# Performance work log

Measured on AMD Instinct MI355X. Metric: run time of the kernel, lower is better.

The kernel has to match this reference:

```python
import jax, jax.numpy as jnp
import numpy as np

NUM_FEATURES = 5
HIDDEN = 64
NUM_CLASSES = 5
N_NODES = 100000
N_EDGES = 1600000


def setup_inputs() -> dict:
    key = jax.random.key(0)
    ks = jax.random.split(key, 8)
    x = jax.random.normal(ks[0], (N_NODES, 4, NUM_FEATURES), dtype=jnp.float32)
    edge_index = jax.random.randint(ks[1], (2, N_EDGES), 0, N_NODES, dtype=jnp.int64)
    batch = jnp.zeros((N_NODES,), dtype=jnp.int64)
    # GCNConv layer 1: 5 -> 64, layer 2: 64 -> 64, output Linear: 64 -> 5
    W1 = jax.random.normal(ks[2], (NUM_FEATURES, HIDDEN), dtype=jnp.float32) / np.sqrt(NUM_FEATURES)
    b1 = jnp.zeros((HIDDEN,), dtype=jnp.float32)
    W2 = jax.random.normal(ks[3], (HIDDEN, HIDDEN), dtype=jnp.float32) / np.sqrt(HIDDEN)
    b2 = jnp.zeros((HIDDEN,), dtype=jnp.float32)
    Wout = jax.random.normal(ks[4], (HIDDEN, NUM_CLASSES), dtype=jnp.float32) / np.sqrt(HIDDEN)
    bout = jnp.zeros((NUM_CLASSES,), dtype=jnp.float32)
    return {"x": x, "edge_index": edge_index, "batch": batch,
            "W1": W1, "b1": b1, "W2": W2, "b2": b2, "Wout": Wout, "bout": bout}


def reference(x, edge_index, batch, W1, b1, W2, b2, Wout, bout):
    N = x.shape[0]
    src, dst = edge_index[0], edge_index[1]
    # GCN symmetric normalization with self-loops: deg counts incoming edges + self loop
    deg = jax.ops.segment_sum(jnp.ones(src.shape, jnp.float32), dst, num_segments=N) + 1.0
    dinv_sqrt = jax.lax.rsqrt(deg)
    norm = dinv_sqrt[src] * dinv_sqrt[dst]            # [E]
    self_norm = (1.0 / deg)[:, None]                  # self-loop weight deg^-1

    def gcn_conv(h, W, b):
        h = h @ W                                     # [N, out]
        agg = jax.ops.segment_sum(h[src] * norm[:, None], dst, num_segments=N)
        return agg + h * self_norm + b

    h = jax.nn.relu(gcn_conv(x[:, -1, :], W1, b1))    # [N, HIDDEN]
    h = jax.nn.relu(gcn_conv(h, W2, b2))              # [N, HIDDEN]
    return jax.nn.softmax(h @ Wout + bout, axis=1)    # [N, 5]
```

## Files before the change

### kernel.cpp

```cpp
#include <hip/hip_runtime.h>
#include <hip/hip_fp16.h>

#define HID 64
#define NF 5
#define NC 5

#define WSH 8
#define WINN 256
#define NBMAX 512
#define SRCB 17
#define NBLK_FILL 160

__global__ void k_zero_i32(int* __restrict__ p, int n) {
    int i = blockIdx.x * blockDim.x + threadIdx.x;
    if (i < n) p[i] = 0;
}


__global__ __launch_bounds__(256) void k_bcount(const int* __restrict__ dst, int E, int chunk,
                                                int nb, int* __restrict__ bcount) {
    __shared__ int cnt[NBMAX];
    for (int i = threadIdx.x; i < nb; i += 256) cnt[i] = 0;
    __syncthreads();
    int c0 = blockIdx.x * chunk;
    int c1 = c0 + chunk; if (c1 > E) c1 = E;
    for (int i = c0 + threadIdx.x; i < c1; i += 256)
        atomicAdd(&cnt[dst[i] >> WSH], 1);
    __syncthreads();
    for (int i = threadIdx.x; i < nb; i += 256) {
        int v = cnt[i];
        if (v) atomicAdd(&bcount[i], v);
    }
}

__global__ __launch_bounds__(512) void k_bscan2(const int* __restrict__ bcount, int nb, int N,
                                                int* __restrict__ bbase, int* __restrict__ bcursor,
                                                int* __restrict__ offsets) {
    __shared__ int s[512];
    int t = threadIdx.x;
    int v = (t < nb) ? bcount[t] : 0;
    s[t] = v;
    __syncthreads();
    for (int o = 1; o < 512; o <<= 1) {
        int u = (t >= o) ? s[t - o] : 0;
        __syncthreads();
        s[t] += u;
        __syncthreads();
    }
    if (t < nb) { bbase[t] = s[t] - v; bcursor[t] = s[t] - v; }
    if (t == nb - 1) { bbase[nb] = s[t]; offsets[N] = s[t]; }
}

__global__ __launch_bounds__(256) void k_bfill(const int* __restrict__ src,
                                               const int* __restrict__ dst, int E, int chunk,
                                               int nb, int* __restrict__ bcursor,
                                               unsigned int* __restrict__ pairbuf) {
    __shared__ int cnt[NBMAX];
    __shared__ int wcur[NBMAX];
    for (int i = threadIdx.x; i < nb; i += 256) cnt[i] = 0;
    __syncthreads();
    int c0 = blockIdx.x * chunk;
    int c1 = c0 + chunk; if (c1 > E) c1 = E;
    for (int i = c0 + threadIdx.x; i < c1; i += 256)
        atomicAdd(&cnt[dst[i] >> WSH], 1);
    __syncthreads();
    for (int i = threadIdx.x; i < nb; i += 256) {
        int v = cnt[i];
        wcur[i] = v ? atomicAdd(&bcursor[i], v) : 0;
    }
    __syncthreads();
    for (int i = c0 + threadIdx.x; i < c1; i += 256) {
        int d = dst[i];
        int b = d >> WSH;
        int p = atomicAdd(&wcur[b], 1);
        pairbuf[p] = ((unsigned)(d & (WINN - 1)) << SRCB) | (unsigned)src[i];
    }
}

__global__ __launch_bounds__(WINN) void k_csr(const unsigned int* __restrict__ pairbuf,
                                              const int* __restrict__ bbase, int N,
                                              const float* __restrict__ x,
                                              int* __restrict__ offsets,
                                              int* __restrict__ csr_src,
                                              float* __restrict__ dinv,
                                              float* __restrict__ xs) {
    int b = blockIdx.x, t = threadIdx.x;
    int winStart = b << WSH;
    int rbeg = bbase[b], rend = bbase[b + 1];
    __shared__ int deg[WINN];
    __shared__ int cur[WINN];
    __shared__ int s[WINN];
    deg[t] = 0;
    __syncthreads();
    for (int p = rbeg + t; p < rend; p += WINN)
        atomicAdd(&deg[pairbuf[p] >> SRCB], 1);
    __syncthreads();
    int v = deg[t];
    s[t] = v;
    __syncthreads();
    for (int o = 1; o < WINN; o <<= 1) {
        int u = (t >= o) ? s[t - o] : 0;
        __syncthreads();
        s[t] += u;
        __syncthreads();
    }
    int node = winStart + t;
    if (node < N) {
        int base = rbeg + s[t] - v;
        offsets[node] = base;
        cur[t] = base;
        float dv = rsqrtf((float)v + 1.0f);
        dinv[node] = dv;
        const float* xr = x + (size_t)node * (4 * NF) + 3 * NF;
#pragma unroll
        for (int k = 0; k < NF; ++k) xs[(size_t)node * NF + k] = xr[k] * dv;
    }
    __syncthreads();
    for (int p = rbeg + t; p < rend; p += WINN) {
        unsigned u = pairbuf[p];
        int dl = u >> SRCB;
        int sn = u & ((1u << SRCB) - 1);
        int pos = atomicAdd(&cur[dl], 1);
        csr_src[pos] = sn;
    }
}


__global__ __launch_bounds__(256) void k_aggX(const float* __restrict__ xs,
                                              const float* __restrict__ W1,
                                              const int* __restrict__ offsets,
                                              const int* __restrict__ csr_src,
                                              const float* __restrict__ dinv,
                                              const float* __restrict__ b1,
                                              __half* __restrict__ g1, int N) {
    int wid = (blockIdx.x * blockDim.x + threadIdx.x) >> 6;
    int lane = threadIdx.x & 63;
    int g = lane >> 3;
    int f = lane & 7;
    float w0 = W1[0 * HID + lane], w1 = W1[1 * HID + lane], w2 = W1[2 * HID + lane],
          w3 = W1[3 * HID + lane], w4 = W1[4 * HID + lane];
    if (wid >= N) return;
    int e0 = offsets[wid], e1 = offsets[wid + 1];
    bool fa = (f < NF);
    float acc = 0.f;
    int ee = e0 + g;
    int s = (ee < e1) ? csr_src[ee] : -1;
    for (int e = e0; e < e1; e += 8) {
        int cs = s;
        int en = e + 8 + g;
        s = (en < e1) ? csr_src[en] : -1;
        if (cs >= 0 && fa) acc += xs[(size_t)cs * NF + f];
    }
    if (g == 0 && fa) acc += xs[(size_t)wid * NF + f];
    acc += __shfl_xor(acc, 8, 64);
    acc += __shfl_xor(acc, 16, 64);
    acc += __shfl_xor(acc, 32, 64);
    float a0 = __shfl(acc, 0, 8), a1 = __shfl(acc, 1, 8), a2 = __shfl(acc, 2, 8),
          a3 = __shfl(acc, 3, 8), a4 = __shfl(acc, 4, 8);
    float dv = dinv[wid];
    float sres = a0 * w0 + a1 * w1 + a2 * w2 + a3 * w3 + a4 * w4;
    float r = fmaxf(fmaf(dv, sres, b1[lane]), 0.f) * dv;
    g1[(size_t)wid * HID + lane] = __float2half(r);
}

__global__ __launch_bounds__(256) void k_aggG(const __half* __restrict__ g1,
                                              const int* __restrict__ offsets,
                                              const int* __restrict__ csr_src,
                                              const float* __restrict__ dinv,
                                              float* __restrict__ aggH, int N) {
    int wid = (blockIdx.x * blockDim.x + threadIdx.x) >> 6;
    if (wid >= N) return;
    int lane = threadIdx.x & 63;
    int g = lane >> 3;
    int f8 = (lane & 7) << 3;
    int e0 = offsets[wid], e1 = offsets[wid + 1];
    float acc[8];
#pragma unroll
    for (int i = 0; i < 8; ++i) acc[i] = 0.f;
    int ee = e0 + g;
    int s = (ee < e1) ? csr_src[ee] : -1;
    for (int e = e0; e < e1; e += 8) {
        int cs = s;
        int en = e + 8 + g;
        s = (en < e1) ? csr_src[en] : -1;
        if (cs >= 0) {
            float4 raw = *reinterpret_cast<const float4*>(g1 + (size_t)cs * HID + f8);
            float2 p0 = __half22float2(*reinterpret_cast<__half2*>(&raw.x));
            float2 p1 = __half22float2(*reinterpret_cast<__half2*>(&raw.y));
            float2 p2 = __half22float2(*reinterpret_cast<__half2*>(&raw.z));
            float2 p3 = __half22float2(*reinterpret_cast<__half2*>(&raw.w));
            acc[0] += p0.x; acc[1] += p0.y; acc[2] += p1.x; acc[3] += p1.y;
            acc[4] += p2.x; acc[5] += p2.y; acc[6] += p3.x; acc[7] += p3.y;
        }
    }
#pragma unroll
    for (int o = 8; o < 64; o <<= 1) {
#pragma unroll
        for (int i = 0; i < 8; ++i) acc[i] += __shfl_xor(acc[i], o, 64);
    }
    if (lane < 8) {
        float4 raw = *reinterpret_cast<const float4*>(g1 + (size_t)wid * HID + f8);
        float2 p0 = __half22float2(*reinterpret_cast<__half2*>(&raw.x));
        float2 p1 = __half22float2(*reinterpret_cast<__half2*>(&raw.y));
        float2 p2 = __half22float2(*reinterpret_cast<__half2*>(&raw.z));
        float2 p3 = __half22float2(*reinterpret_cast<__half2*>(&raw.w));
        float dv = dinv[wid];
        float4 r0, r1;
        r0.x = dv * (acc[0] + p0.x); r0.y = dv * (acc[1] + p0.y);
        r0.z = dv * (acc[2] + p1.x); r0.w = dv * (acc[3] + p1.y);
        r1.x = dv * (acc[4] + p2.x); r1.y = dv * (acc[5] + p2.y);
        r1.z = dv * (acc[6] + p3.x); r1.w = dv * (acc[7] + p3.y);
        float4* dst4 = reinterpret_cast<float4*>(aggH + (size_t)wid * HID + f8);
        dst4[0] = r0;
        dst4[1] = r1;
    }
}

__global__ __launch_bounds__(256) void k_fuse(const float* __restrict__ aggH,
                                              const float* __restrict__ W2,
                                              const float* __restrict__ b2,
                                              const float* __restrict__ Wout,
                                              const float* __restrict__ bout,
                                              float* __restrict__ out, int N) {
    __shared__ float4 sh4[64][17];
    __shared__ float4 sW4[64 * 16];
    __shared__ float  swout[64][NC];
    __shared__ float  sb2[64];
    __shared__ float  sbout[8];
    int tx = threadIdx.x;
    int nb0 = blockIdx.x * 64;

    const float4* W2_4 = reinterpret_cast<const float4*>(W2);
    for (int i = tx; i < 64 * 16; i += 256) sW4[i] = W2_4[i];
    const float4* aggH4 = reinterpret_cast<const float4*>(aggH);
    for (int i = tx; i < 64 * 16; i += 256) {
        int row = i >> 4, c4 = i & 15;
        int node = nb0 + row;
        float4 v = {0.f, 0.f, 0.f, 0.f};
        if (node < N) v = aggH4[(size_t)node * 16 + c4];
        sh4[row][c4] = v;
    }
    if (tx < 64) sb2[tx] = b2[tx];
    for (int i = tx; i < 64 * NC; i += 256) swout[i / NC][i % NC] = Wout[i];
    if (tx < NC) sbout[tx] = bout[tx];
    __syncthreads();

    int ty = tx >> 4;
    int txl = tx & 15;

    float acc[4][4];
#pragma unroll
    for (int j = 0; j < 4; ++j)
#pragma unroll
        for (int i = 0; i < 4; ++i) acc[j][i] = 0.f;

    for (int k4 = 0; k4 < 16; ++k4) {
        float4 w0 = sW4[(k4 * 4 + 0) * 16 + txl];
        float4 w1 = sW4[(k4 * 4 + 1) * 16 + txl];
        float4 w2 = sW4[(k4 * 4 + 2) * 16 + txl];
        float4 w3 = sW4[(k4 * 4 + 3) * 16 + txl];
#pragma unroll
        for (int j = 0; j < 4; ++j) {
            float4 hq = sh4[ty * 4 + j][k4];
            acc[j][0] = fmaf(hq.x, w0.x, fmaf(hq.y, w1.x, fmaf(hq.z, w2.x, fmaf(hq.w, w3.x, acc[j][0]))));
            acc[j][1] = fmaf(hq.x, w0.y, fmaf(hq.y, w1.y, fmaf(hq.z, w2.y, fmaf(hq.w, w3.y, acc[j][1]))));
            acc[j][2] = fmaf(hq.x, w0.z, fmaf(hq.y, w1.z, fmaf(hq.z, w2.z, fmaf(hq.w, w3.z, acc[j][2]))));
            acc[j][3] = fmaf(hq.x, w0.w, fmaf(hq.y, w1.w, fmaf(hq.z, w2.w, fmaf(hq.w, w3.w, acc[j][3]))));
        }
    }

    float pl[4][NC];
#pragma unroll
    for (int j = 0; j < 4; ++j)
#pragma unroll
        for (int c = 0; c < NC; ++c) pl[j][c] = 0.f;
#pragma unroll
    for (int j = 0; j < 4; ++j) {
#pragma unroll
        for (int i = 0; i < 4; ++i) {
            int f = txl * 4 + i;
            float h2 = fmaxf(acc[j][i] + sb2[f], 0.f);
#pragma unroll
            for (int c = 0; c < NC; ++c) pl[j][c] = fmaf(h2, swout[f][c], pl[j][c]);
        }
    }
#pragma unroll
    for (int o = 1; o < 16; o <<= 1) {
#pragma unroll
        for (int j = 0; j < 4; ++j)
#pragma unroll
            for (int c = 0; c < NC; ++c) pl[j][c] += __shfl_xor(pl[j][c], o, 64);
    }
    if (txl == 0) {
#pragma unroll
        for (int j = 0; j < 4; ++j) {
            int node = nb0 + ty * 4 + j;
            if (node < N) {
                float lg[NC];
#pragma unroll
                for (int c = 0; c < NC; ++c) lg[c] = pl[j][c] + sbout[c];
                float m = lg[0];
#pragma unroll
                for (int c = 1; c < NC; ++c) m = fmaxf(m, lg[c]);
                float ssum = 0.f, ex[NC];
#pragma unroll
                for (int c = 0; c < NC; ++c) { ex[c] = __expf(lg[c] - m); ssum += ex[c]; }
                float inv = 1.0f / ssum;
#pragma unroll
                for (int c = 0; c < NC; ++c) out[(size_t)node * NC + c] = ex[c] * inv;
            }
        }
    }
}


extern "C" void kernel_launch(void* const* d_in, const int* in_sizes, int n_in,
                              void* d_out, int out_size, void* d_ws, size_t ws_size,
                              hipStream_t stream) {
    const float* x   = (const float*)d_in[0];
    const int*   ei  = (const int*)d_in[1];
    const float* W1  = (const float*)d_in[3];
    const float* b1  = (const float*)d_in[4];
    const float* W2  = (const float*)d_in[5];
    const float* b2  = (const float*)d_in[6];
    const float* Wo  = (const float*)d_in[7];
    const float* bo  = (const float*)d_in[8];
    float* out = (float*)d_out;

    const int N = in_sizes[2];
    const int E = in_sizes[1] / 2;

    size_t off = 0;
    char* base = (char*)d_ws;
    auto alloc = [&](size_t bytes) -> void* {
        off = (off + 255) & ~(size_t)255;
        void* r = base + off;
        off += bytes;
        return r;
    };
    int*      bcount  = (int*)alloc((size_t)NBMAX * 4);
    int*      bbase   = (int*)alloc(((size_t)NBMAX + 1) * 4);
    int*      bcursor = (int*)alloc((size_t)NBMAX * 4);
    unsigned* pairbuf = (unsigned*)alloc((size_t)E * 4);
    int*      offsets = (int*)alloc(((size_t)N + 1) * 4);
    int*      csr_src = (int*)alloc((size_t)E * 4);
    float*    dinv    = (float*)alloc((size_t)N * 4);
    float*    xs      = (float*)alloc((size_t)N * NF * 4);
    __half*   g1      = (__half*)alloc((size_t)N * HID * 2);
    float*    aggH    = (float*)alloc((size_t)N * HID * 4);

    const int T = 256;
    int gNF = ((N * HID) + T - 1) / T;

    const int* src = ei;
    const int* dst = ei + E;

    int nb = (N + WINN - 1) >> WSH;
    int chunk = (E + NBLK_FILL - 1) / NBLK_FILL;

    k_zero_i32<<<(nb + 255) / 256, 256, 0, stream>>>(bcount, nb);
    k_bcount<<<NBLK_FILL, 256, 0, stream>>>(dst, E, chunk, nb, bcount);
    k_bscan2<<<1, 512, 0, stream>>>(bcount, nb, N, bbase, bcursor, offsets);
    k_bfill<<<NBLK_FILL, 256, 0, stream>>>(src, dst, E, chunk, nb, bcursor, pairbuf);
    k_csr<<<nb, WINN, 0, stream>>>(pairbuf, bbase, N, x, offsets, csr_src, dinv, xs);

    k_aggX<<<gNF, T, 0, stream>>>(xs, W1, offsets, csr_src, dinv, b1, g1, N);

    k_aggG<<<gNF, T, 0, stream>>>(g1, offsets, csr_src, dinv, aggH, N);

    int nbF = (N + 63) / 64;
    k_fuse<<<nbF, 256, 0, stream>>>(aggH, W2, b2, Wo, bo, out, N);
}
```

Measured before the change: 244.6 us.

## Replace atomic bucket cursors with per-block count matrix and scan; widen windows

The bucket sort that builds the CSR now writes each block's per-bucket counts to a count matrix. A new column-wise scan kernel turns these into deterministic write offsets, so the fill pass no longer recounts the edges and no longer uses global atomics or a zero-init kernel. The window size also goes from 256 to 512 nodes, halving the number of buckets and doubling the k_csr block size. The cost is an extra kernel launch and the count-matrix traffic, and the larger windows change load balance and shared-memory usage in k_csr.

```diff
diff --git a/kernel.cpp b/kernel.cpp
--- a/kernel.cpp
+++ b/kernel.cpp
@@ -5,71 +5,77 @@
 #define NF 5
 #define NC 5
 
-#define WSH 8
-#define WINN 256
-#define NBMAX 512
+#define WSH 9
+#define WINN 512
+#define NBMAX 256
 #define SRCB 17
-#define NBLK_FILL 160
-
-__global__ void k_zero_i32(int* __restrict__ p, int n) {
-    int i = blockIdx.x * blockDim.x + threadIdx.x;
-    if (i < n) p[i] = 0;
-}
-
-
-__global__ __launch_bounds__(256) void k_bcount(const int* __restrict__ dst, int E, int chunk,
-                                                int nb, int* __restrict__ bcount) {
+#define NBLK 256
+
+
+__global__ __launch_bounds__(512) void k_bcount(const int* __restrict__ dst, int E, int chunk,
+                                                int nb, int* __restrict__ cntmat) {
     __shared__ int cnt[NBMAX];
-    for (int i = threadIdx.x; i < nb; i += 256) cnt[i] = 0;
+    int t = threadIdx.x;
+    for (int i = t; i < nb; i += 512) cnt[i] = 0;
     __syncthreads();
     int c0 = blockIdx.x * chunk;
     int c1 = c0 + chunk; if (c1 > E) c1 = E;
-    for (int i = c0 + threadIdx.x; i < c1; i += 256)
+    for (int i = c0 + t; i < c1; i += 512)
         atomicAdd(&cnt[dst[i] >> WSH], 1);
     __syncthreads();
-    for (int i = threadIdx.x; i < nb; i += 256) {
-        int v = cnt[i];
-        if (v) atomicAdd(&bcount[i], v);
-    }
-}
-
-__global__ __launch_bounds__(512) void k_bscan2(const int* __restrict__ bcount, int nb, int N,
-                                                int* __restrict__ bbase, int* __restrict__ bcursor,
+    for (int i = t; i < nb; i += 512) cntmat[blockIdx.x * nb + i] = cnt[i];
+}
+
+__global__ __launch_bounds__(NBLK) void k_wscan(int* __restrict__ cntmat, int nb,
+                                                int* __restrict__ btot) {
+    __shared__ int s[NBLK];
+    int b = blockIdx.x;
+    int t = threadIdx.x;
+    int v = cntmat[t * nb + b];
+    s[t] = v;
+    __syncthreads();
+    for (int o = 1; o < NBLK; o <<= 1) {
+        int u = (t >= o) ? s[t - o] : 0;
+        __syncthreads();
+        s[t] += u;
+        __syncthreads();
+    }
+    cntmat[t * nb + b] = s[t] - v;
+    if (t == NBLK - 1) btot[b] = s[t];
+}
+
+__global__ __launch_bounds__(256) void k_bscan2(const int* __restrict__ btot, int nb, int N,
+                                                int* __restrict__ bbase,
                                                 int* __restrict__ offsets) {
-    __shared__ int s[512];
+    __shared__ int s[256];
     int t = threadIdx.x;
-    int v = (t < nb) ? bcount[t] : 0;
+    int v = (t < nb) ? btot[t] : 0;
     s[t] = v;
     __syncthreads();
-    for (int o = 1; o < 512; o <<= 1) {
+    for (int o = 1; o < 256; o <<= 1) {
         int u = (t >= o) ? s[t - o] : 0;
         __syncthreads();
         s[t] += u;
         __syncthreads();
     }
-    if (t < nb) { bbase[t] = s[t] - v; bcursor[t] = s[t] - v; }
+    if (t < nb) bbase[t] = s[t] - v;
     if (t == nb - 1) { bbase[nb] = s[t]; offsets[N] = s[t]; }
 }
 
-__global__ __launch_bounds__(256) void k_bfill(const int* __restrict__ src,
+__global__ __launch_bounds__(512) void k_bfill(const int* __restrict__ src,
                                                const int* __restrict__ dst, int E, int chunk,
-                                               int nb, int* __restrict__ bcursor,
+                                               int nb, const int* __restrict__ bbase,
+                                               const int* __restrict__ cntmat,
                                                unsigned int* __restrict__ pairbuf) {
-    __shared__ int cnt[NBMAX];
     __shared__ int wcur[NBMAX];
-    for (int i = threadIdx.x; i < nb; i += 256) cnt[i] = 0;
-    __syncthreads();
-    int c0 = blockIdx.x * chunk;
+    int t = threadIdx.x;
+    int blk = blockIdx.x;
+    for (int i = t; i < nb; i += 512)
+        wcur[i] = bbase[i] + cntmat[blk * nb + i];
+    __syncthreads();
+    int c0 = blk * chunk;
     int c1 = c0 + chunk; if (c1 > E) c1 = E;
-    for (int i = c0 + threadIdx.x; i < c1; i += 256)
-        atomicAdd(&cnt[dst[i] >> WSH], 1);
-    __syncthreads();
-    for (int i = threadIdx.x; i < nb; i += 256) {
-        int v = cnt[i];
-        wcur[i] = v ? atomicAdd(&bcursor[i], v) : 0;
-    }
-    __syncthreads();
-    for (int i = c0 + threadIdx.x; i < c1; i += 256) {
+    for (int i = c0 + t; i < c1; i += 512) {
         int d = dst[i];
         int b = d >> WSH;
         int p = atomicAdd(&wcur[b], 1);
@@ -338,9 +344,9 @@
         off += bytes;
         return r;
     };
-    int*      bcount  = (int*)alloc((size_t)NBMAX * 4);
+    int*      cntmat  = (int*)alloc((size_t)NBLK * NBMAX * 4);
+    int*      btot    = (int*)alloc((size_t)NBMAX * 4);
     int*      bbase   = (int*)alloc(((size_t)NBMAX + 1) * 4);
-    int*      bcursor = (int*)alloc((size_t)NBMAX * 4);
     unsigned* pairbuf = (unsigned*)alloc((size_t)E * 4);
     int*      offsets = (int*)alloc(((size_t)N + 1) * 4);
     int*      csr_src = (int*)alloc((size_t)E * 4);
@@ -356,12 +362,12 @@
     const int* dst = ei + E;
 
     int nb = (N + WINN - 1) >> WSH;
-    int chunk = (E + NBLK_FILL - 1) / NBLK_FILL;
-
-    k_zero_i32<<<(nb + 255) / 256, 256, 0, stream>>>(bcount, nb);
-    k_bcount<<<NBLK_FILL, 256, 0, stream>>>(dst, E, chunk, nb, bcount);
-    k_bscan2<<<1, 512, 0, stream>>>(bcount, nb, N, bbase, bcursor, offsets);
-    k_bfill<<<NBLK_FILL, 256, 0, stream>>>(src, dst, E, chunk, nb, bcursor, pairbuf);
+    int chunk = (E + NBLK - 1) / NBLK;
+
+    k_bcount<<<NBLK, 512, 0, stream>>>(dst, E, chunk, nb, cntmat);
+    k_wscan<<<nb, NBLK, 0, stream>>>(cntmat, nb, btot);
+    k_bscan2<<<1, 256, 0, stream>>>(btot, nb, N, bbase, offsets);
+    k_bfill<<<NBLK, 512, 0, stream>>>(src, dst, E, chunk, nb, bbase, cntmat, pairbuf);
     k_csr<<<nb, WINN, 0, stream>>>(pairbuf, bbase, N, x, offsets, csr_src, dinv, xs);
 
     k_aggX<<<gNF, T, 0, stream>>>(xs, W1, offsets, csr_src, dinv, b1, g1, N);
```

After: 218.9 us. -10.5%, faster.
